# Kernel optimization log

Hardware: AMD Instinct MI355X
Metric: run time of the kernel (lower is better)

The kernel has to match this reference:

```python
import jax, jax.numpy as jnp
import numpy as np

B, T, C = 4, 2048, 1024
H = 16
D = C // H  # head_dim = 64

def setup_inputs() -> dict:
    key = jax.random.key(0)
    ks = jax.random.split(key, 5)
    scale = 0.02
    x = jax.random.normal(ks[0], (B, T, C), dtype=jnp.float32)
    # weights stored [in, out] (transpose of torch Linear layout; same math)
    Wqkv = jax.random.normal(ks[1], (C, 3 * C), dtype=jnp.float32) * scale
    bqkv = jnp.zeros((3 * C,), dtype=jnp.float32)
    Wproj = jax.random.normal(ks[2], (C, C), dtype=jnp.float32) * scale
    bproj = jnp.zeros((C,), dtype=jnp.float32)
    return {"x": x, "Wqkv": Wqkv, "bqkv": bqkv, "Wproj": Wproj, "bproj": bproj}

def reference(x, Wqkv, bqkv, Wproj, bproj):
    Bx, Tx, Cx = x.shape
    qkv = x @ Wqkv + bqkv                      # [B,T,3C]
    q, k, v = jnp.split(qkv, 3, axis=2)
    # [B,T,C] -> [B,H,T,D]
    q = q.reshape(Bx, Tx, H, D).transpose(0, 2, 1, 3)
    k = k.reshape(Bx, Tx, H, D).transpose(0, 2, 1, 3)
    v = v.reshape(Bx, Tx, H, D).transpose(0, 2, 1, 3)
    att = jnp.einsum('bhqd,bhkd->bhqk', q, k) / jnp.sqrt(jnp.float32(D))
    causal = jnp.tril(jnp.ones((Tx, Tx), dtype=bool))
    att = jnp.where(causal, att, jnp.float32(-jnp.inf))
    att = jax.nn.softmax(att, axis=-1)
    y = jnp.einsum('bhqk,bhkd->bhqd', att, v)  # [B,H,T,D]
    y = y.transpose(0, 2, 1, 3).reshape(Bx, Tx, Cx)
    return y @ Wproj + bproj
```

## Files before the change

### kernel.cpp

```cpp
#include <hip/hip_runtime.h>
#include <math.h>

#define Bb 4
#define Tt 2048
#define Cc 1024
#define Hh 16
#define Dd 64
#define QSC 0.18033688011112042f

typedef unsigned short ushort_t;
typedef __attribute__((ext_vector_type(8))) short short8;
typedef __attribute__((ext_vector_type(4))) float floatx4;

typedef unsigned int __attribute__((address_space(1))) u32_as1;
typedef unsigned int __attribute__((address_space(3))) u32_as3;

__device__ __forceinline__ void gld_lds16(const void* g, const void* lds_uniform) {
    __builtin_amdgcn_global_load_lds(
        (const u32_as1*)(unsigned long long)g,
        (u32_as3*)(unsigned int)(unsigned long long)lds_uniform,
        16, 0, 0);
}

__device__ inline ushort_t f2bf(float x) {
    unsigned int u = __float_as_uint(x);
    return (ushort_t)((u + 0x7FFFu + ((u >> 16) & 1u)) >> 16);
}

__device__ __forceinline__ void bar() {
    asm volatile("" ::: "memory");
    __builtin_amdgcn_s_barrier();
    asm volatile("" ::: "memory");
}

__global__ __launch_bounds__(256) void convert_kernel(
    const float* __restrict__ in, ushort_t* __restrict__ out, int n4)
{
    int i = blockIdx.x * 256 + threadIdx.x;
    if (i < n4) {
        float4 v = *(const float4*)&in[i * 4];
        ushort_t o[4] = {f2bf(v.x), f2bf(v.y), f2bf(v.z), f2bf(v.w)};
        *(uint2*)&out[i * 4] = *(uint2*)o;
    }
}

__global__ __launch_bounds__(256) void transpose_kernel(
    const float* __restrict__ W, ushort_t* __restrict__ Wt, int K, int N)
{
    __shared__ ushort_t Ts[16][72];
    const int n0 = blockIdx.x * 64;
    const int k0 = blockIdx.y * 16;
    const int t = threadIdx.x;
#pragma unroll
    for (int i = 0; i < 4; i++) {
        int e = t + i * 256;
        int kl = e >> 6, nl = e & 63;
        Ts[kl][nl] = f2bf(W[(size_t)(k0 + kl) * N + n0 + nl]);
    }
    __syncthreads();
    {
        int nl = t >> 2, kl4 = (t & 3) * 4;
        ushort_t o[4] = {Ts[kl4][nl], Ts[kl4 + 1][nl], Ts[kl4 + 2][nl], Ts[kl4 + 3][nl]};
        *(uint2*)&Wt[(size_t)(n0 + nl) * K + k0 + kl4] = *(uint2*)o;
    }
}

template <bool OUT_BF16, bool SCALE_Q>
__global__ __launch_bounds__(512) void gemm256_kernel(
    const ushort_t* __restrict__ A, const ushort_t* __restrict__ Bt,
    const float* __restrict__ bias, void* __restrict__ Co,
    int M, int N, int K)
{
    __shared__ __align__(16) ushort_t Ls[65536];

    const int tid = threadIdx.x;
    const int lane = tid & 63;
    const int w = tid >> 6;
    const int wm = w >> 2, wn = w & 3;
    const int l = lane & 15, q = lane >> 4;
    const int NT = K >> 6;

    const int n0 = blockIdx.x * 256;
    const int m0 = blockIdx.y * 256;

    const int ln = lane ^ (((lane >> 5) & 1) << 1);
    const ushort_t* Ag = A  + (size_t)(m0 + w * 16 + (ln >> 2)) * K + (ln & 3) * 8;
    const ushort_t* Bg = Bt + (size_t)(n0 + w * 16 + (ln >> 2)) * K + (ln & 3) * 8;

    const int swz = l * 32 + ((q * 8) ^ (((l >> 3) & 1) << 4));

    floatx4 acc[2][2][4][2];
#pragma unroll
    for (int qm = 0; qm < 2; qm++)
#pragma unroll
        for (int qn = 0; qn < 2; qn++)
#pragma unroll
            for (int mf = 0; mf < 4; mf++)
#pragma unroll
                for (int nf = 0; nf < 2; nf++)
                    acc[qm][qn][mf][nf] = (floatx4){0.f, 0.f, 0.f, 0.f};

    short8 af[4][2], bf0[2][2], bf1[2][2];

#define STAGE_(SLOT, MAT, HALF, T, GB) {                                        \
    const ushort_t* _g = (GB) + (size_t)(HALF) * 128 * K + (size_t)(T) * 64;    \
    const ushort_t* _l = &Ls[(SLOT) * 32768 + (MAT) * 16384 + (HALF) * 8192 + w * 1024]; \
    gld_lds16(_g, _l);                                                          \
    gld_lds16(_g + 32, _l + 512); }
#define STAGE_A(SLOT, HALF, T) STAGE_((SLOT), 0, (HALF), (T), Ag)
#define STAGE_B(SLOT, HALF, T) STAGE_((SLOT), 1, (HALF), (T), Bg)

#define LDA(SLOT, QM) {                                                         \
    _Pragma("unroll") for (int mf = 0; mf < 4; mf++)                            \
    _Pragma("unroll") for (int kc = 0; kc < 2; kc++)                            \
        af[mf][kc] = *(const short8*)&Ls[(SLOT) * 32768 + (QM) * 8192 +         \
            ((wm * 4 + mf) * 2 + kc) * 512 + swz]; }

#define LDB(SLOT, QN, DST) {                                                    \
    _Pragma("unroll") for (int nf = 0; nf < 2; nf++)                            \
    _Pragma("unroll") for (int kc = 0; kc < 2; kc++)                            \
        DST[nf][kc] = *(const short8*)&Ls[(SLOT) * 32768 + 16384 + (QN) * 8192 + \
            ((wn * 2 + nf) * 2 + kc) * 512 + swz]; }

#define MM(QM, QN, BF) {                                                        \
    __builtin_amdgcn_s_setprio(1);                                              \
    _Pragma("unroll") for (int kc = 0; kc < 2; kc++)                            \
    _Pragma("unroll") for (int mf = 0; mf < 4; mf++)                            \
    _Pragma("unroll") for (int nf = 0; nf < 2; nf++)                            \
        acc[QM][QN][mf][nf] = __builtin_amdgcn_mfma_f32_16x16x32_bf16(          \
            af[mf][kc], BF[nf][kc], acc[QM][QN][mf][nf], 0, 0, 0);              \
    __builtin_amdgcn_s_setprio(0); }

#define LGKM0() asm volatile("s_waitcnt lgkmcnt(0)" ::: "memory")

    STAGE_A(0, 0, 0); STAGE_B(0, 0, 0); STAGE_B(0, 1, 0); STAGE_A(0, 1, 0);
    if (NT > 1) {
        STAGE_A(1, 0, 1); STAGE_B(1, 0, 1); STAGE_B(1, 1, 1);
        asm volatile("s_waitcnt vmcnt(6)" ::: "memory");
    } else {
        asm volatile("s_waitcnt vmcnt(0)" ::: "memory");
    }
    bar();

    for (int g = 0; g < NT; ++g) {
        const int slot = g & 1;

        LDA(slot, 0);
        LDB(slot, 0, bf0);
        if (g + 1 < NT) STAGE_A(slot ^ 1, 1, g + 1);
        bar();
        LGKM0();
        MM(0, 0, bf0);
        bar();

        LDB(slot, 1, bf1);
        if (g + 2 < NT) STAGE_A(slot, 0, g + 2);
        bar();
        LGKM0();
        MM(0, 1, bf1);
        bar();

        LDA(slot, 1);
        if (g + 2 < NT) STAGE_B(slot, 0, g + 2);
        bar();
        LGKM0();
        MM(1, 1, bf1);
        bar();

        if (g + 2 < NT) STAGE_B(slot, 1, g + 2);
        bar();
        LGKM0();
        MM(1, 0, bf0);
        if (g + 1 < NT) {
            if (g + 2 < NT) asm volatile("s_waitcnt vmcnt(6)" ::: "memory");
            else            asm volatile("s_waitcnt vmcnt(0)" ::: "memory");
            bar();
        }
    }

#pragma unroll
    for (int qn = 0; qn < 2; qn++)
#pragma unroll
        for (int nf = 0; nf < 2; nf++) {
            const int col = n0 + qn * 128 + wn * 32 + nf * 16 + l;
            const float bi = bias[col];
            const float sc = (SCALE_Q && col < 1024) ? QSC : 1.0f;
#pragma unroll
            for (int qm = 0; qm < 2; qm++)
#pragma unroll
                for (int mf = 0; mf < 4; mf++)
#pragma unroll
                    for (int r = 0; r < 4; r++) {
                        const int row = m0 + qm * 128 + wm * 64 + mf * 16 + q * 4 + r;
                        const float v = (acc[qm][qn][mf][nf][r] + bi) * sc;
                        if (OUT_BF16)
                            ((ushort_t*)Co)[(size_t)row * N + col] = f2bf(v);
                        else
                            ((float*)Co)[(size_t)row * N + col] = v;
                    }
        }
#undef STAGE_
#undef STAGE_A
#undef STAGE_B
#undef LDA
#undef LDB
#undef MM
#undef LGKM0
}

__device__ __forceinline__ int ks_swz(int I) {
    return I ^ (((I >> 8) & 1) * 0x28) ^ (((I >> 9) & 1) * 0x10);
}
__device__ __forceinline__ int vt_idx(int row, int col) {
    return row * 80 + (col ^ ((((row >> 2) ^ (row >> 4)) & 3) << 3));
}
__device__ __forceinline__ int ps_idx(int row, int col) {
    return row * 80 + (col ^ (((row >> 2) & 3) << 3));
}

#define KS_SLOT 4096
#define VT_SLOT 6400

__global__ __launch_bounds__(256, 2) void attn_mfma_kernel(
    const ushort_t* __restrict__ qkv, ushort_t* __restrict__ yatt)
{
    __shared__ __align__(16) ushort_t Ks[2 * KS_SLOT];
    __shared__ __align__(16) ushort_t Vt[2 * VT_SLOT];
    __shared__ __align__(16) ushort_t Ps[4][16 * 80];

    const int tid = threadIdx.x;
    const int lane = tid & 63;
    const int w = tid >> 6;
    const int quad = lane >> 4;
    const int l = lane & 15;

    const int bh = blockIdx.x;
    const int j = 15 - (int)blockIdx.y;
    const int q0 = j * 128;
    const int b = bh >> 4;
    const int h = bh & 15;
    const size_t base = (size_t)b * Tt * (3 * Cc);
    const int qoff = h * 64;
    const int koff = Cc + h * 64;
    const int voff = 2 * Cc + h * 64;

    for (int i = tid; i < 16 * 64; i += 256) {
        const int vi = vt_idx(64 + i / 64, i % 64);
        Vt[vi] = 0x3F80;
        Vt[VT_SLOT + vi] = 0x3F80;
    }

    short8 Qf[2][2];
#pragma unroll
    for (int mt = 0; mt < 2; mt++)
#pragma unroll
        for (int kc = 0; kc < 2; kc++)
            Qf[mt][kc] = *(const short8*)&qkv[base
                + (size_t)(q0 + mt * 64 + w * 16 + l) * (3 * Cc)
                + qoff + kc * 32 + quad * 8];

    floatx4 Oacc[2][4];
    floatx4 Lacc[2];
#pragma unroll
    for (int mt = 0; mt < 2; mt++) {
        Lacc[mt] = (floatx4){0.f, 0.f, 0.f, 0.f};
#pragma unroll
        for (int dt = 0; dt < 4; dt++)
            Oacc[mt][dt] = (floatx4){0.f, 0.f, 0.f, 0.f};
    }

    const int srow = tid >> 2;
    const int sd0 = (tid & 3) * 16;
    const int knt = srow >> 4, kl = srow & 15;
    const int kc_s = sd0 >> 5;
    const int qp0 = (sd0 & 31) >> 3;
    const int pcol = (srow & 15) * 4 + (srow >> 4);

    const int ntil = 2 * j + 2;

    const ushort_t* kp0 = &qkv[base + (size_t)srow * (3 * Cc) + koff + sd0];
    const ushort_t* vp0 = &qkv[base + (size_t)srow * (3 * Cc) + voff + sd0];

    const int ksw0 = ks_swz((knt * 2 + kc_s) * 512 + (qp0 * 16 + kl) * 8);
    const int ksw1 = ks_swz((knt * 2 + kc_s) * 512 + ((qp0 + 1) * 16 + kl) * 8);

    uint4 pk0 = *(const uint4*)kp0;
    uint4 pk1 = *(const uint4*)(kp0 + 8);
    uint4 pv0 = *(const uint4*)vp0;
    uint4 pv1 = *(const uint4*)(vp0 + 8);

#define WRITE_TILE(SLOT) {                                                      \
    *(uint4*)&Ks[(SLOT) * KS_SLOT + ksw0] = pk0;                                \
    *(uint4*)&Ks[(SLOT) * KS_SLOT + ksw1] = pk1;                                \
    ushort_t tv[16];                                                            \
    *(uint4*)&tv[0] = pv0;                                                      \
    *(uint4*)&tv[8] = pv1;                                                      \
    _Pragma("unroll") for (int t2 = 0; t2 < 16; t2++)                           \
        Vt[(SLOT) * VT_SLOT + vt_idx(sd0 + t2, pcol)] = tv[t2]; }

#define LOAD_TILE(KT) {                                                         \
    const size_t _off = (size_t)((KT) * 64) * (3 * Cc);                         \
    pk0 = *(const uint4*)(kp0 + _off);                                          \
    pk1 = *(const uint4*)(kp0 + _off + 8);                                      \
    pv0 = *(const uint4*)(vp0 + _off);                                          \
    pv1 = *(const uint4*)(vp0 + _off + 8); }

    WRITE_TILE(0);
    if (ntil > 1) LOAD_TILE(1);
    __syncthreads();

    for (int kt = 0; kt < ntil; kt++) {
        const int kbase = kt * 64;
        const int slot = kt & 1;

        short8 Vf[5][2];
#pragma unroll
        for (int dt = 0; dt < 5; dt++)
#pragma unroll
            for (int kc = 0; kc < 2; kc++)
                Vf[dt][kc] = *(const short8*)&Vt[slot * VT_SLOT
                    + vt_idx(dt * 16 + l, kc * 32 + quad * 8)];

        if (kt + 1 < ntil) {
            WRITE_TILE(slot ^ 1);
            if (kt + 2 < ntil) LOAD_TILE(kt + 2);
        }

#pragma unroll
        for (int mt = 0; mt < 2; mt++) {
            const int qmin = q0 + mt * 64 + (w << 4);
            if (kbase > qmin + 15) continue;

            floatx4 S[4];
#pragma unroll
            for (int nt = 0; nt < 4; nt++) S[nt] = (floatx4){0.f, 0.f, 0.f, 0.f};
            __builtin_amdgcn_s_setprio(1);
#pragma unroll
            for (int kc = 0; kc < 2; kc++) {
#pragma unroll
                for (int nt = 0; nt < 4; nt++) {
                    short8 kf = *(const short8*)&Ks[slot * KS_SLOT
                        + ks_swz((nt * 2 + kc) * 512 + lane * 8)];
                    S[nt] = __builtin_amdgcn_mfma_f32_16x16x32_bf16(
                        Qf[mt][kc], kf, S[nt], 0, 0, 0);
                }
            }
            __builtin_amdgcn_s_setprio(0);

            const bool need_mask = (kbase + 63 > qmin);

#pragma unroll
            for (int r = 0; r < 4; r++) {
                const int qrow = qmin + quad * 4 + r;
                float e[4];
#pragma unroll
                for (int nt = 0; nt < 4; nt++) {
                    float s2 = S[nt][r];
                    if (need_mask && (kbase + nt * 16 + l > qrow)) s2 = -INFINITY;
                    e[nt] = __builtin_amdgcn_exp2f(s2);
                }
                unsigned int u0 = __builtin_amdgcn_perm(
                    __float_as_uint(e[1]), __float_as_uint(e[0]), 0x07060302u);
                unsigned int u1 = __builtin_amdgcn_perm(
                    __float_as_uint(e[3]), __float_as_uint(e[2]), 0x07060302u);
                uint2 pk; pk.x = u0; pk.y = u1;
                *(uint2*)&Ps[w][ps_idx(quad * 4 + r, l * 4)] = pk;
            }
            asm volatile("" ::: "memory");

            short8 Pa0 = *(const short8*)&Ps[w][ps_idx(l, quad * 8)];
            short8 Pa1 = *(const short8*)&Ps[w][ps_idx(l, 32 + quad * 8)];
            __builtin_amdgcn_s_setprio(1);
#pragma unroll
            for (int dt = 0; dt < 4; dt++) {
                Oacc[mt][dt] = __builtin_amdgcn_mfma_f32_16x16x32_bf16(
                    Pa0, Vf[dt][0], Oacc[mt][dt], 0, 0, 0);
                Oacc[mt][dt] = __builtin_amdgcn_mfma_f32_16x16x32_bf16(
                    Pa1, Vf[dt][1], Oacc[mt][dt], 0, 0, 0);
            }
            Lacc[mt] = __builtin_amdgcn_mfma_f32_16x16x32_bf16(
                Pa0, Vf[4][0], Lacc[mt], 0, 0, 0);
            Lacc[mt] = __builtin_amdgcn_mfma_f32_16x16x32_bf16(
                Pa1, Vf[4][1], Lacc[mt], 0, 0, 0);
            __builtin_amdgcn_s_setprio(0);
            asm volatile("" ::: "memory");
        }

        __syncthreads();
    }

#pragma unroll
    for (int mt = 0; mt < 2; mt++)
#pragma unroll
        for (int r = 0; r < 4; r++) {
            const float rl = 1.f / Lacc[mt][r];
            const int qrow = q0 + mt * 64 + (w << 4) + quad * 4 + r;
#pragma unroll
            for (int dt = 0; dt < 4; dt++)
                yatt[(size_t)(b * Tt + qrow) * Cc + h * 64 + dt * 16 + l] =
                    f2bf(Oacc[mt][dt][r] * rl);
        }
#undef WRITE_TILE
#undef LOAD_TILE
}

extern "C" void kernel_launch(void* const* d_in, const int* in_sizes, int n_in,
                              void* d_out, int out_size, void* d_ws, size_t ws_size,
                              hipStream_t stream) {
    const float* x     = (const float*)d_in[0];
    const float* Wqkv  = (const float*)d_in[1];
    const float* bqkv  = (const float*)d_in[2];
    const float* Wproj = (const float*)d_in[3];
    const float* bproj = (const float*)d_in[4];
    float* out = (float*)d_out;

    ushort_t* qkvb   = (ushort_t*)d_ws;
    ushort_t* yattb  = qkvb + (size_t)8192 * 3072;
    ushort_t* xb     = yattb + (size_t)8192 * 1024;
    ushort_t* wqkvt  = xb + (size_t)8192 * 1024;
    ushort_t* wprojt = wqkvt + (size_t)3072 * 1024;

    convert_kernel<<<(8192 * 1024 / 4 + 255) / 256, 256, 0, stream>>>(x, xb, 8192 * 1024 / 4);
    transpose_kernel<<<dim3(3072 / 64, 1024 / 16), 256, 0, stream>>>(Wqkv, wqkvt, 1024, 3072);
    transpose_kernel<<<dim3(1024 / 64, 1024 / 16), 256, 0, stream>>>(Wproj, wprojt, 1024, 1024);

    gemm256_kernel<true, true><<<dim3(3072 / 256, 8192 / 256), 512, 0, stream>>>(
        xb, wqkvt, bqkv, qkvb, 8192, 3072, 1024);
    attn_mfma_kernel<<<dim3(64, 16), 256, 0, stream>>>(qkvb, yattb);
    gemm256_kernel<false, false><<<dim3(1024 / 256, 8192 / 256), 512, 0, stream>>>(
        yattb, wprojt, bproj, out, 8192, 1024, 1024);
}
```

Before: 269.6 us.

## Shrink GEMM M-tile to 128 and interleave two query tiles in attention

```diff
diff --git a/kernel.cpp b/kernel.cpp
--- a/kernel.cpp
+++ b/kernel.cpp
@@ -66,12 +66,12 @@
 }
 
 template <bool OUT_BF16, bool SCALE_Q>
-__global__ __launch_bounds__(512) void gemm256_kernel(
+__global__ __launch_bounds__(512) void gemm128_kernel(
     const ushort_t* __restrict__ A, const ushort_t* __restrict__ Bt,
     const float* __restrict__ bias, void* __restrict__ Co,
     int M, int N, int K)
 {
-    __shared__ __align__(16) ushort_t Ls[65536];
+    __shared__ __align__(16) ushort_t Ls[49152];
 
     const int tid = threadIdx.x;
     const int lane = tid & 63;
@@ -81,7 +81,7 @@
     const int NT = K >> 6;
 
     const int n0 = blockIdx.x * 256;
-    const int m0 = blockIdx.y * 256;
+    const int m0 = blockIdx.y * 128;
 
     const int ln = lane ^ (((lane >> 5) & 1) << 1);
     const ushort_t* Ag = A  + (size_t)(m0 + w * 16 + (ln >> 2)) * K + (ln & 3) * 8;
@@ -89,54 +89,55 @@
 
     const int swz = l * 32 + ((q * 8) ^ (((l >> 3) & 1) << 4));
 
-    floatx4 acc[2][2][4][2];
-#pragma unroll
-    for (int qm = 0; qm < 2; qm++)
-#pragma unroll
-        for (int qn = 0; qn < 2; qn++)
-#pragma unroll
-            for (int mf = 0; mf < 4; mf++)
-#pragma unroll
-                for (int nf = 0; nf < 2; nf++)
-                    acc[qm][qn][mf][nf] = (floatx4){0.f, 0.f, 0.f, 0.f};
+    floatx4 acc[2][4][2];
+#pragma unroll
+    for (int qn = 0; qn < 2; qn++)
+#pragma unroll
+        for (int mf = 0; mf < 4; mf++)
+#pragma unroll
+            for (int nf = 0; nf < 2; nf++)
+                acc[qn][mf][nf] = (floatx4){0.f, 0.f, 0.f, 0.f};
 
     short8 af[4][2], bf0[2][2], bf1[2][2];
 
-#define STAGE_(SLOT, MAT, HALF, T, GB) {                                        \
-    const ushort_t* _g = (GB) + (size_t)(HALF) * 128 * K + (size_t)(T) * 64;    \
-    const ushort_t* _l = &Ls[(SLOT) * 32768 + (MAT) * 16384 + (HALF) * 8192 + w * 1024]; \
+#define STAGE_A(SLOT, T) {                                                      \
+    const ushort_t* _g = Ag + (size_t)(T) * 64;                                 \
+    const ushort_t* _l = &Ls[(SLOT) * 24576 + w * 1024];                        \
     gld_lds16(_g, _l);                                                          \
     gld_lds16(_g + 32, _l + 512); }
-#define STAGE_A(SLOT, HALF, T) STAGE_((SLOT), 0, (HALF), (T), Ag)
-#define STAGE_B(SLOT, HALF, T) STAGE_((SLOT), 1, (HALF), (T), Bg)
-
-#define LDA(SLOT, QM) {                                                         \
+#define STAGE_B(SLOT, H, T) {                                                   \
+    const ushort_t* _g = Bg + (size_t)(H) * 128 * K + (size_t)(T) * 64;         \
+    const ushort_t* _l = &Ls[(SLOT) * 24576 + (1 + (H)) * 8192 + w * 1024];     \
+    gld_lds16(_g, _l);                                                          \
+    gld_lds16(_g + 32, _l + 512); }
+
+#define LDA(SLOT) {                                                             \
     _Pragma("unroll") for (int mf = 0; mf < 4; mf++)                            \
     _Pragma("unroll") for (int kc = 0; kc < 2; kc++)                            \
-        af[mf][kc] = *(const short8*)&Ls[(SLOT) * 32768 + (QM) * 8192 +         \
+        af[mf][kc] = *(const short8*)&Ls[(SLOT) * 24576 +                       \
             ((wm * 4 + mf) * 2 + kc) * 512 + swz]; }
 
 #define LDB(SLOT, QN, DST) {                                                    \
     _Pragma("unroll") for (int nf = 0; nf < 2; nf++)                            \
     _Pragma("unroll") for (int kc = 0; kc < 2; kc++)                            \
-        DST[nf][kc] = *(const short8*)&Ls[(SLOT) * 32768 + 16384 + (QN) * 8192 + \
+        DST[nf][kc] = *(const short8*)&Ls[(SLOT) * 24576 + (1 + (QN)) * 8192 +  \
             ((wn * 2 + nf) * 2 + kc) * 512 + swz]; }
 
-#define MM(QM, QN, BF) {                                                        \
+#define MM(QN, BF) {                                                            \
     __builtin_amdgcn_s_setprio(1);                                              \
     _Pragma("unroll") for (int kc = 0; kc < 2; kc++)                            \
     _Pragma("unroll") for (int mf = 0; mf < 4; mf++)                            \
     _Pragma("unroll") for (int nf = 0; nf < 2; nf++)                            \
-        acc[QM][QN][mf][nf] = __builtin_amdgcn_mfma_f32_16x16x32_bf16(          \
-            af[mf][kc], BF[nf][kc], acc[QM][QN][mf][nf], 0, 0, 0);              \
+        acc[QN][mf][nf] = __builtin_amdgcn_mfma_f32_16x16x32_bf16(              \
+            af[mf][kc], BF[nf][kc], acc[QN][mf][nf], 0, 0, 0);                  \
     __builtin_amdgcn_s_setprio(0); }
 
 #define LGKM0() asm volatile("s_waitcnt lgkmcnt(0)" ::: "memory")
 
-    STAGE_A(0, 0, 0); STAGE_B(0, 0, 0); STAGE_B(0, 1, 0); STAGE_A(0, 1, 0);
+    STAGE_A(0, 0); STAGE_B(0, 0, 0); STAGE_B(0, 1, 0);
     if (NT > 1) {
-        STAGE_A(1, 0, 1); STAGE_B(1, 0, 1); STAGE_B(1, 1, 1);
-        asm volatile("s_waitcnt vmcnt(6)" ::: "memory");
+        STAGE_A(1, 1); STAGE_B(1, 0, 1);
+        asm volatile("s_waitcnt vmcnt(4)" ::: "memory");
     } else {
         asm volatile("s_waitcnt vmcnt(0)" ::: "memory");
     }
@@ -145,34 +146,21 @@
     for (int g = 0; g < NT; ++g) {
         const int slot = g & 1;
 
-        LDA(slot, 0);
+        LDA(slot);
         LDB(slot, 0, bf0);
-        if (g + 1 < NT) STAGE_A(slot ^ 1, 1, g + 1);
+        if (g + 1 < NT) STAGE_B(slot ^ 1, 1, g + 1);
         bar();
         LGKM0();
-        MM(0, 0, bf0);
+        MM(0, bf0);
         bar();
 
         LDB(slot, 1, bf1);
-        if (g + 2 < NT) STAGE_A(slot, 0, g + 2);
+        if (g + 2 < NT) { STAGE_A(slot, g + 2); STAGE_B(slot, 0, g + 2); }
         bar();
         LGKM0();
-        MM(0, 1, bf1);
-        bar();
-
-        LDA(slot, 1);
-        if (g + 2 < NT) STAGE_B(slot, 0, g + 2);
-        bar();
-        LGKM0();
-        MM(1, 1, bf1);
-        bar();
-
-        if (g + 2 < NT) STAGE_B(slot, 1, g + 2);
-        bar();
-        LGKM0();
-        MM(1, 0, bf0);
+        MM(1, bf1);
         if (g + 1 < NT) {
-            if (g + 2 < NT) asm volatile("s_waitcnt vmcnt(6)" ::: "memory");
+            if (g + 2 < NT) asm volatile("s_waitcnt vmcnt(4)" ::: "memory");
             else            asm volatile("s_waitcnt vmcnt(0)" ::: "memory");
             bar();
         }
@@ -186,20 +174,17 @@
             const float bi = bias[col];
             const float sc = (SCALE_Q && col < 1024) ? QSC : 1.0f;
 #pragma unroll
-            for (int qm = 0; qm < 2; qm++)
-#pragma unroll
-                for (int mf = 0; mf < 4; mf++)
-#pragma unroll
-                    for (int r = 0; r < 4; r++) {
-                        const int row = m0 + qm * 128 + wm * 64 + mf * 16 + q * 4 + r;
-                        const float v = (acc[qm][qn][mf][nf][r] + bi) * sc;
-                        if (OUT_BF16)
-                            ((ushort_t*)Co)[(size_t)row * N + col] = f2bf(v);
-                        else
-                            ((float*)Co)[(size_t)row * N + col] = v;
-                    }
+            for (int mf = 0; mf < 4; mf++)
+#pragma unroll
+                for (int r = 0; r < 4; r++) {
+                    const int row = m0 + wm * 64 + mf * 16 + q * 4 + r;
+                    const float v = (acc[qn][mf][nf][r] + bi) * sc;
+                    if (OUT_BF16)
+                        ((ushort_t*)Co)[(size_t)row * N + col] = f2bf(v);
+                    else
+                        ((float*)Co)[(size_t)row * N + col] = v;
+                }
         }
-#undef STAGE_
 #undef STAGE_A
 #undef STAGE_B
 #undef LDA
@@ -226,7 +211,7 @@
 {
     __shared__ __align__(16) ushort_t Ks[2 * KS_SLOT];
     __shared__ __align__(16) ushort_t Vt[2 * VT_SLOT];
-    __shared__ __align__(16) ushort_t Ps[4][16 * 80];
+    __shared__ __align__(16) ushort_t Ps[4][2 * 1280];
 
     const int tid = threadIdx.x;
     const int lane = tid & 63;
@@ -305,6 +290,40 @@
     pv0 = *(const uint4*)(vp0 + _off);                                          \
     pv1 = *(const uint4*)(vp0 + _off + 8); }
 
+#define SOFTMAX(SV, MT) {                                                       \
+    const int qminX = q0 + (MT) * 64 + (w << 4);                                \
+    const bool needm = (kbase + 63 > qminX);                                    \
+    _Pragma("unroll") for (int r = 0; r < 4; r++) {                             \
+        const int qrow = qminX + quad * 4 + r;                                  \
+        float e[4];                                                             \
+        _Pragma("unroll") for (int nt = 0; nt < 4; nt++) {                      \
+            float s2 = SV[nt][r];                                               \
+            if (needm && (kbase + nt * 16 + l > qrow)) s2 = -INFINITY;          \
+            e[nt] = __builtin_amdgcn_exp2f(s2);                                 \
+        }                                                                       \
+        unsigned int u0 = __builtin_amdgcn_perm(                                \
+            __float_as_uint(e[1]), __float_as_uint(e[0]), 0x07060302u);         \
+        unsigned int u1 = __builtin_amdgcn_perm(                                \
+            __float_as_uint(e[3]), __float_as_uint(e[2]), 0x07060302u);         \
+        uint2 pq; pq.x = u0; pq.y = u1;                                         \
+        *(uint2*)&Ps[w][(MT) * 1280 + ps_idx(quad * 4 + r, l * 4)] = pq; } }
+
+#define PVACC(MT) {                                                             \
+    short8 Pa0 = *(const short8*)&Ps[w][(MT) * 1280 + ps_idx(l, quad * 8)];     \
+    short8 Pa1 = *(const short8*)&Ps[w][(MT) * 1280 + ps_idx(l, 32 + quad * 8)];\
+    __builtin_amdgcn_s_setprio(1);                                              \
+    _Pragma("unroll") for (int dt = 0; dt < 4; dt++) {                          \
+        Oacc[MT][dt] = __builtin_amdgcn_mfma_f32_16x16x32_bf16(                 \
+            Pa0, Vf[dt][0], Oacc[MT][dt], 0, 0, 0);                             \
+        Oacc[MT][dt] = __builtin_amdgcn_mfma_f32_16x16x32_bf16(                 \
+            Pa1, Vf[dt][1], Oacc[MT][dt], 0, 0, 0);                             \
+    }                                                                           \
+    Lacc[MT] = __builtin_amdgcn_mfma_f32_16x16x32_bf16(                         \
+        Pa0, Vf[4][0], Lacc[MT], 0, 0, 0);                                      \
+    Lacc[MT] = __builtin_amdgcn_mfma_f32_16x16x32_bf16(                         \
+        Pa1, Vf[4][1], Lacc[MT], 0, 0, 0);                                      \
+    __builtin_amdgcn_s_setprio(0); }
+
     WRITE_TILE(0);
     if (ntil > 1) LOAD_TILE(1);
     __syncthreads();
@@ -326,65 +345,46 @@
             if (kt + 2 < ntil) LOAD_TILE(kt + 2);
         }
 
-#pragma unroll
-        for (int mt = 0; mt < 2; mt++) {
-            const int qmin = q0 + mt * 64 + (w << 4);
-            if (kbase > qmin + 15) continue;
-
-            floatx4 S[4];
-#pragma unroll
-            for (int nt = 0; nt < 4; nt++) S[nt] = (floatx4){0.f, 0.f, 0.f, 0.f};
-            __builtin_amdgcn_s_setprio(1);
-#pragma unroll
-            for (int kc = 0; kc < 2; kc++) {
+        const int qmin0 = q0 + (w << 4);
+        const bool act0 = (kbase <= qmin0 + 15);
+
+        floatx4 S1[4], S0[4];
+#pragma unroll
+        for (int nt = 0; nt < 4; nt++) S1[nt] = (floatx4){0.f, 0.f, 0.f, 0.f};
+        __builtin_amdgcn_s_setprio(1);
+        if (act0) {
+#pragma unroll
+            for (int nt = 0; nt < 4; nt++) S0[nt] = (floatx4){0.f, 0.f, 0.f, 0.f};
+#pragma unroll
+            for (int kc = 0; kc < 2; kc++)
 #pragma unroll
                 for (int nt = 0; nt < 4; nt++) {
                     short8 kf = *(const short8*)&Ks[slot * KS_SLOT
                         + ks_swz((nt * 2 + kc) * 512 + lane * 8)];
-                    S[nt] = __builtin_amdgcn_mfma_f32_16x16x32_bf16(
-                        Qf[mt][kc], kf, S[nt], 0, 0, 0);
+                    S1[nt] = __builtin_amdgcn_mfma_f32_16x16x32_bf16(
+                        Qf[1][kc], kf, S1[nt], 0, 0, 0);
+                    S0[nt] = __builtin_amdgcn_mfma_f32_16x16x32_bf16(
+                        Qf[0][kc], kf, S0[nt], 0, 0, 0);
                 }
-            }
-            __builtin_amdgcn_s_setprio(0);
-
-            const bool need_mask = (kbase + 63 > qmin);
-
-#pragma unroll
-            for (int r = 0; r < 4; r++) {
-                const int qrow = qmin + quad * 4 + r;
-                float e[4];
+        } else {
+#pragma unroll
+            for (int kc = 0; kc < 2; kc++)
 #pragma unroll
                 for (int nt = 0; nt < 4; nt++) {
-                    float s2 = S[nt][r];
-                    if (need_mask && (kbase + nt * 16 + l > qrow)) s2 = -INFINITY;
-                    e[nt] = __builtin_amdgcn_exp2f(s2);
+                    short8 kf = *(const short8*)&Ks[slot * KS_SLOT
+                        + ks_swz((nt * 2 + kc) * 512 + lane * 8)];
+                    S1[nt] = __builtin_amdgcn_mfma_f32_16x16x32_bf16(
+                        Qf[1][kc], kf, S1[nt], 0, 0, 0);
                 }
-                unsigned int u0 = __builtin_amdgcn_perm(
-                    __float_as_uint(e[1]), __float_as_uint(e[0]), 0x07060302u);
-                unsigned int u1 = __builtin_amdgcn_perm(
-                    __float_as_uint(e[3]), __float_as_uint(e[2]), 0x07060302u);
-                uint2 pk; pk.x = u0; pk.y = u1;
-                *(uint2*)&Ps[w][ps_idx(quad * 4 + r, l * 4)] = pk;
-            }
-            asm volatile("" ::: "memory");
-
-            short8 Pa0 = *(const short8*)&Ps[w][ps_idx(l, quad * 8)];
-            short8 Pa1 = *(const short8*)&Ps[w][ps_idx(l, 32 + quad * 8)];
-            __builtin_amdgcn_s_setprio(1);
-#pragma unroll
-            for (int dt = 0; dt < 4; dt++) {
-                Oacc[mt][dt] = __builtin_amdgcn_mfma_f32_16x16x32_bf16(
-                    Pa0, Vf[dt][0], Oacc[mt][dt], 0, 0, 0);
-                Oacc[mt][dt] = __builtin_amdgcn_mfma_f32_16x16x32_bf16(
-                    Pa1, Vf[dt][1], Oacc[mt][dt], 0, 0, 0);
-            }
-            Lacc[mt] = __builtin_amdgcn_mfma_f32_16x16x32_bf16(
-                Pa0, Vf[4][0], Lacc[mt], 0, 0, 0);
-            Lacc[mt] = __builtin_amdgcn_mfma_f32_16x16x32_bf16(
-                Pa1, Vf[4][1], Lacc[mt], 0, 0, 0);
-            __builtin_amdgcn_s_setprio(0);
-            asm volatile("" ::: "memory");
         }
+        __builtin_amdgcn_s_setprio(0);
+
+        SOFTMAX(S1, 1);
+        if (act0) SOFTMAX(S0, 0);
+        asm volatile("" ::: "memory");
+
+        PVACC(1);
+        if (act0) PVACC(0);
 
         __syncthreads();
     }
@@ -402,6 +402,8 @@
         }
 #undef WRITE_TILE
 #undef LOAD_TILE
+#undef SOFTMAX
+#undef PVACC
 }
 
 extern "C" void kernel_launch(void* const* d_in, const int* in_sizes, int n_in,
@@ -424,9 +426,9 @@
     transpose_kernel<<<dim3(3072 / 64, 1024 / 16), 256, 0, stream>>>(Wqkv, wqkvt, 1024, 3072);
     transpose_kernel<<<dim3(1024 / 64, 1024 / 16), 256, 0, stream>>>(Wproj, wprojt, 1024, 1024);
 
-    gemm256_kernel<true, true><<<dim3(3072 / 256, 8192 / 256), 512, 0, stream>>>(
+    gemm128_kernel<true, true><<<dim3(3072 / 256, 8192 / 128), 512, 0, stream>>>(
         xb, wqkvt, bqkv, qkvb, 8192, 3072, 1024);
     attn_mfma_kernel<<<dim3(64, 16), 256, 0, stream>>>(qkvb, yattb);
-    gemm256_kernel<false, false><<<dim3(1024 / 256, 8192 / 256), 512, 0, stream>>>(
+    gemm128_kernel<false, false><<<dim3(1024 / 256, 8192 / 128), 512, 0, stream>>>(
         yattb, wprojt, bproj, out, 8192, 1024, 1024);
 }
```

New measurement: 256.8 us. 4.7% less time.
